# Kernel tuning notes

Measured on AMD Instinct MI355X. Metric: run time of the kernel, lower is better.

Reference implementation:

```python
import jax, jax.numpy as jnp
import numpy as np

D = 4
P_PIX = 13   # 2*R+1, R=6
R_PIX = 6
P_REG = 7    # R+1
DIRATE = 2   # min(4, (20-0)//15 + 1) for ref_index=[0,18], current_ind=20, dil_int=15


def correlate(t, r, P, d):
    """SpatialCorrelationSampler(kernel_size=1, patch_size=P, dilation_patch=d).
    t, r: [b,c,h,w] -> [b,P*P,h,w] ; corr[n=(i*P+j)] uses r shifted by ((i-R)*d,(j-R)*d)."""
    b, c, h, w = t.shape
    Rr = (P - 1) // 2
    pad = Rr * d
    rp = jnp.pad(r, ((0, 0), (0, 0), (pad, pad), (pad, pad)))
    # [b,c,N,h,w] stack of shifted views (zero-padded borders)
    shifts = jnp.stack([rp[:, :, i * d:i * d + h, j * d:j * d + w]
                        for i in range(P) for j in range(P)], axis=2)
    return jnp.einsum('bcyx,bcnyx->bnyx', t, shifts)


def deform_im2col(r, offset, P):
    """Deformable im2col with one shared (x,y) offset per output pixel.
    r: [b,c,h,w], offset: [b,h,w,2] (x in [...,0], y in [...,1]) -> [b,c,P*P,h,w].
    Bilinear sampling with zero outside the image."""
    b, c, h, w = r.shape
    Rr = (P - 1) // 2
    N = P * P
    ky, kx = jnp.meshgrid(jnp.arange(-Rr, Rr + 1), jnp.arange(-Rr, Rr + 1), indexing='ij')
    ky = ky.reshape(-1).astype(r.dtype)
    kx = kx.reshape(-1).astype(r.dtype)
    ys = jnp.arange(h, dtype=r.dtype)
    xs = jnp.arange(w, dtype=r.dtype)
    sy = offset[..., 1][:, None] + ys[None, None, :, None] + ky[None, :, None, None]  # [b,N,h,w]
    sx = offset[..., 0][:, None] + xs[None, None, None, :] + kx[None, :, None, None]
    y0 = jnp.floor(sy)
    x0 = jnp.floor(sx)
    wy = sy - y0
    wx = sx - x0
    rf = r.reshape(b, c, h * w)

    def gather(yi, xi):
        valid = ((yi >= 0) & (yi < h) & (xi >= 0) & (xi < w)).astype(r.dtype)
        idx = (jnp.clip(yi, 0, h - 1).astype(jnp.int32) * w
               + jnp.clip(xi, 0, w - 1).astype(jnp.int32)).reshape(b, 1, -1)
        vals = jnp.take_along_axis(rf, jnp.broadcast_to(idx, (b, c, N * h * w)), axis=2)
        return vals.reshape(b, c, N, h, w), valid

    v00, m00 = gather(y0, x0)
    v01, m01 = gather(y0, x0 + 1)
    v10, m10 = gather(y0 + 1, x0)
    v11, m11 = gather(y0 + 1, x0 + 1)
    w00 = ((1 - wy) * (1 - wx) * m00)[:, None]
    w01 = ((1 - wy) * wx * m01)[:, None]
    w10 = (wy * (1 - wx) * m10)[:, None]
    w11 = (wy * wx * m11)[:, None]
    return v00 * w00 + v01 * w01 + v10 * w10 + v11 * w11


def unfold(x, P):
    """F.unfold(x, kernel_size=P, padding=(P-1)//2) -> [b,c,P*P,h,w]."""
    b, c, h, w = x.shape
    Rr = (P - 1) // 2
    xp = jnp.pad(x, ((0, 0), (0, 0), (Rr, Rr), (Rr, Rr)))
    return jnp.stack([xp[:, :, i:i + h, j:j + w]
                      for i in range(P) for j in range(P)], axis=2)


def setup_inputs() -> dict:
    key = jax.random.key(0)
    ks = jax.random.split(key, 8)
    inp = {
        'feats_r0': jax.random.normal(ks[0], (2, 128, 32, 32), jnp.float32),
        'feats_r1': jax.random.normal(ks[1], (2, 128, 32, 32), jnp.float32),
        'feats_t': jax.random.normal(ks[2], (2, 128, 32, 32), jnp.float32),
        'quantized_r0': jax.random.uniform(ks[3], (2, 3, 128, 128), jnp.float32),
        'quantized_r1': jax.random.uniform(ks[4], (2, 3, 128, 128), jnp.float32),
        'feats_r_semantic0': jax.random.normal(ks[5], (2, 512, 16, 16), jnp.float32),
        'feats_r_semantic1': jax.random.normal(ks[6], (2, 512, 16, 16), jnp.float32),
        'feats_t_semantic': jax.random.normal(ks[7], (2, 512, 16, 16), jnp.float32),
        'current_ind': 20,
    }
    return inp


def reference(feats_r0, feats_r1, feats_t, quantized_r0, quantized_r1,
              feats_r_semantic0, feats_r_semantic1, feats_t_semantic, current_ind):
    b, c, h, w = feats_t.shape
    b_, c_, h_, w_ = feats_t_semantic.shape
    P, Rr, N = P_PIX, R_PIX, P_PIX * P_PIX

    # --- searching ref 0 (far in time): dilated coarse correlation -> soft offset ---
    coarse = correlate(feats_t, feats_r0, P, DIRATE)                     # [b,N,h,w]
    cs = jax.nn.softmax(coarse.reshape(b, N, h * w), axis=1).reshape(b, P, P, h, w)
    gv = jnp.arange(-Rr, Rr + 1, dtype=feats_t.dtype)
    off_x = jnp.einsum('bijyx,j->byx', cs, gv) * DIRATE
    off_y = jnp.einsum('bijyx,i->byx', cs, gv) * DIRATE
    offset = jnp.stack([off_x, off_y], axis=-1)                          # [b,h,w,2]

    col0 = deform_im2col(feats_r0, offset, P)                            # [b,c,N,h,w]
    corr0 = jnp.einsum('bcyx,bcnyx->bnyx', feats_t, col0).reshape(b, N, h * w)

    # --- recent ref 1: plain pixel + region correlation ---
    corr1 = correlate(feats_t, feats_r1, P, 1).reshape(b, N, h * w)
    region = correlate(feats_t_semantic, feats_r_semantic1, P_REG, 1).reshape(b_, P_REG * P_REG, h_ * w_)
    corr = jax.nn.softmax(region, axis=1)[:, None]                       # [b,1,49,h_*w_]

    corr_pixel = jax.nn.softmax(jnp.concatenate([corr0, corr1], axis=1), axis=1)[:, None]  # [b,1,2N,hw]

    # --- propagate colors ---
    qr0 = quantized_r0[:, :, ::D, ::D]
    qr1 = quantized_r1[:, :, ::D, ::D]
    uf0 = deform_im2col(qr0, offset, P).reshape(b, 3, N, h * w)
    uf1 = unfold(qr1, P).reshape(b, 3, N, h * w)
    image_uf = jnp.concatenate([uf0, uf1], axis=2)                       # [b,3,2N,hw]
    out = (corr_pixel * image_uf).sum(2).reshape(b, 3, h, w)
    return (out, corr)
```

## Files before the change

### kernel.cpp

```cpp
#include <hip/hip_runtime.h>
#include <math.h>

#define HH 32
#define WW 32
#define CC 128
#define PPIX 13
#define RPIX 6
#define NPIX 169
#define G14 14
#define NG 196
#define NTOT 338
#define DIRATE_ 2
#define HS 16
#define WSz 16
#define CS 512
#define PREG 7
#define RREG 3
#define NREG 49
#define QH 128
#define MAIN_BLOCKS 2048
#define REG_BLOCKS 512

__device__ __forceinline__ float wave_sum(float v) {
    #pragma unroll
    for (int s = 1; s < 64; s <<= 1) v += __shfl_xor(v, s, 64);
    return v;
}
__device__ __forceinline__ float wave_max(float v) {
    #pragma unroll
    for (int s = 1; s < 64; s <<= 1) v = fmaxf(v, __shfl_xor(v, s, 64));
    return v;
}

__global__ __launch_bounds__(256) void prep(
    const float* __restrict__ fr0, const float* __restrict__ fr1,
    const float* __restrict__ ft,  const float* __restrict__ qr0,
    const float* __restrict__ qr1, const float* __restrict__ rs1,
    const float* __restrict__ ts,
    float* __restrict__ Tr0, float* __restrict__ Tr1, float* __restrict__ Tt,
    float* __restrict__ Trs1, float* __restrict__ Tts,
    float* __restrict__ qs0, float* __restrict__ qs1)
{
    __shared__ float tile[32][33];
    const int tid = threadIdx.x;
    const int tx = tid & 31, ty = tid >> 5;
    int bid = blockIdx.x;
    if (bid < 768) {
        const int t = bid >> 8, rem = bid & 255;
        const int p0 = (rem & 31) * 32;
        const int c0 = ((rem >> 5) & 3) * 32;
        const int b  = rem >> 7;
        const float* s = (t==0 ? fr0 : t==1 ? fr1 : ft) + (size_t)b*CC*1024;
        float* d       = (t==0 ? Tr0 : t==1 ? Tr1 : Tt) + (size_t)b*CC*1024;
        #pragma unroll
        for (int i = ty; i < 32; i += 8) tile[i][tx] = s[(size_t)(c0+i)*1024 + p0+tx];
        __syncthreads();
        #pragma unroll
        for (int i = ty; i < 32; i += 8) d[(size_t)(p0+i)*CC + c0+tx] = tile[tx][i];
    } else if (bid < 1280) {
        bid -= 768;
        const int t = bid >> 8, rem = bid & 255;
        const int p0 = (rem & 7) * 32;
        const int c0 = ((rem >> 3) & 15) * 32;
        const int b  = rem >> 7;
        const float* s = (t==0 ? rs1 : ts) + (size_t)b*CS*256;
        float* d       = (t==0 ? Trs1 : Tts) + (size_t)b*CS*256;
        #pragma unroll
        for (int i = ty; i < 32; i += 8) tile[i][tx] = s[(size_t)(c0+i)*256 + p0+tx];
        __syncthreads();
        #pragma unroll
        for (int i = ty; i < 32; i += 8) d[(size_t)(p0+i)*CS + c0+tx] = tile[tx][i];
    } else {
        const int base = (bid - 1280) * 256 + tid;
        for (int e = base; e < 2*6144; e += 2048) {
            const int t = e / 6144, r2 = e % 6144;
            const int bc = r2 >> 10, yx = r2 & 1023;
            const int yy = yx >> 5, xx = yx & 31;
            const float v = (t==0 ? qr0 : qr1)[((size_t)bc*QH + yy*4)*QH + xx*4];
            (t==0 ? qs0 : qs1)[r2] = v;
        }
    }
}

__global__ __launch_bounds__(256) void colorizer_fused(
    const float* __restrict__ Tr0,
    const float* __restrict__ Tr1,
    const float* __restrict__ Tt,
    const float* __restrict__ qs0,
    const float* __restrict__ qs1,
    const float* __restrict__ Trs1,
    const float* __restrict__ Tts,
    float* __restrict__ out,
    float* __restrict__ corr_out)
{
    __shared__ __align__(16) float tvec[CS];
    __shared__ float rbuf[40];
    __shared__ float smC0[NPIX];
    __shared__ float smG[NG];
    __shared__ float smC1[NPIX];
    __shared__ float smV[NTOT];
    __shared__ float smQ0[3*NG];
    __shared__ float smQ1[3*NPIX];

    const int tid  = threadIdx.x;
    const int lane = tid & 63;
    const int wid  = tid >> 6;

    if (blockIdx.x < MAIN_BLOCKS) {
        const int b   = blockIdx.x >> 10;
        const int pix = blockIdx.x & 1023;
        const int y = pix >> 5, x = pix & 31;

        if (tid < 32)
            ((float4*)tvec)[tid] = ((const float4*)Tt)[(size_t)b*32768 + pix*32 + tid];
        __syncthreads();

        const float4* tp  = (const float4*)tvec;
        const float4* Tr0q = (const float4*)Tr0 + (size_t)b*32768;
        const float4* Tr1q = (const float4*)Tr1 + (size_t)b*32768;
        const int q4 = lane & 3, g4 = lane >> 2;

        #pragma unroll
        for (int set = 0; set < 3; ++set) {
            const int di = set*64 + wid*16 + g4;
            int inb = 0, yx = 0;
            if (di < NPIX) {
                const int ys = y + (di/PPIX - RPIX)*DIRATE_;
                const int xs = x + (di%PPIX - RPIX)*DIRATE_;
                inb = (ys>=0 && ys<HH && xs>=0 && xs<WW);
                yx = inb ? ys*WW+xs : 0;
            }
            const float4* rp = Tr0q + yx*32 + q4;
            float4 a; a.x=a.y=a.z=a.w=0.f;
            #pragma unroll
            for (int r = 0; r < 8; ++r) {
                const float4 rv = rp[r*4];
                const float4 tv = tp[q4 + r*4];
                a.x = fmaf(rv.x,tv.x,a.x); a.y = fmaf(rv.y,tv.y,a.y);
                a.z = fmaf(rv.z,tv.z,a.z); a.w = fmaf(rv.w,tv.w,a.w);
            }
            float s = (a.x+a.y)+(a.z+a.w);
            s += __shfl_xor(s, 1, 64); s += __shfl_xor(s, 2, 64);
            if (q4 == 0 && di < NPIX) smC0[di] = inb ? s : 0.f;
        }
        __syncthreads();

        const float dv = (tid < NPIX) ? smC0[tid] : 0.f;
        {
            float wm = wave_max(tid < NPIX ? dv : -INFINITY);
            if (lane == 0) rbuf[wid] = wm;
        }
        __syncthreads();
        const float M1 = fmaxf(fmaxf(rbuf[0], rbuf[1]), fmaxf(rbuf[2], rbuf[3]));
        {
            const float e   = (tid < NPIX) ? __expf(dv - M1) : 0.f;
            const float gvj = (tid < NPIX) ? (float)(tid % PPIX - RPIX) : 0.f;
            const float gvi = (tid < NPIX) ? (float)(tid / PPIX - RPIX) : 0.f;
            float s0 = wave_sum(e), s1 = wave_sum(e*gvj), s2 = wave_sum(e*gvi);
            if (lane == 0) { rbuf[4+wid] = s0; rbuf[8+wid] = s1; rbuf[12+wid] = s2; }
        }
        __syncthreads();
        const float ssum = rbuf[4]+rbuf[5]+rbuf[6]+rbuf[7];
        const float sx   = rbuf[8]+rbuf[9]+rbuf[10]+rbuf[11];
        const float sy   = rbuf[12]+rbuf[13]+rbuf[14]+rbuf[15];
        const float off_x = sx / ssum * (float)DIRATE_;
        const float off_y = sy / ssum * (float)DIRATE_;

        const float fy = (float)y + off_y, fx = (float)x + off_x;
        const float fly = floorf(fy), flx = floorf(fx);
        const int yb = (int)fly - RPIX, xb = (int)flx - RPIX;
        const float wy = fy - fly, wx = fx - flx;
        const float w00 = (1.f-wy)*(1.f-wx), w01 = (1.f-wy)*wx;
        const float w10 = wy*(1.f-wx),       w11 = wy*wx;

        #pragma unroll
        for (int set = 0; set < 6; ++set) {
            const int di = set*64 + wid*16 + g4;
            const float4* basep = Tr0q;
            int inb = 0, yx = 0;
            if (di < NG) {
                const int ys = yb + di/G14, xs = xb + di%G14;
                inb = (ys>=0 && ys<HH && xs>=0 && xs<WW);
                yx = inb ? ys*WW+xs : 0;
            } else if (di < NG+NPIX) {
                const int k = di - NG;
                const int ys = y + k/PPIX - RPIX, xs = x + k%PPIX - RPIX;
                inb = (ys>=0 && ys<HH && xs>=0 && xs<WW);
                yx = inb ? ys*WW+xs : 0;
                basep = Tr1q;
            }
            const float4* rp = basep + yx*32 + q4;
            float4 a; a.x=a.y=a.z=a.w=0.f;
            #pragma unroll
            for (int r = 0; r < 8; ++r) {
                const float4 rv = rp[r*4];
                const float4 tv = tp[q4 + r*4];
                a.x = fmaf(rv.x,tv.x,a.x); a.y = fmaf(rv.y,tv.y,a.y);
                a.z = fmaf(rv.z,tv.z,a.z); a.w = fmaf(rv.w,tv.w,a.w);
            }
            float s = (a.x+a.y)+(a.z+a.w);
            s += __shfl_xor(s, 1, 64); s += __shfl_xor(s, 2, 64);
            if (q4 == 0 && di < NG+NPIX) {
                if (di < NG) smG[di] = inb ? s : 0.f;
                else         smC1[di-NG] = inb ? s : 0.f;
            }
        }
        for (int idx = tid; idx < 3*NG; idx += 256) {
            const int ch = idx / NG, a2 = idx % NG;
            const int ys = yb + a2 / G14, xs = xb + a2 % G14;
            smQ0[idx] = (ys>=0 && ys<HH && xs>=0 && xs<WW)
                        ? qs0[(b*3+ch)*1024 + ys*WW + xs] : 0.f;
        }
        for (int idx = tid; idx < 3*NPIX; idx += 256) {
            const int ch = idx / NPIX, a2 = idx % NPIX;
            const int ys = y + a2 / PPIX - RPIX, xs = x + a2 % PPIX - RPIX;
            smQ1[idx] = (ys>=0 && ys<HH && xs>=0 && xs<WW)
                        ? qs1[(b*3+ch)*1024 + ys*WW + xs] : 0.f;
        }
        __syncthreads();

        for (int idx = tid; idx < NTOT; idx += 256) {
            float v;
            if (idx < NPIX) {
                const int i = idx / PPIX, j = idx % PPIX;
                const int g = i*G14 + j;
                v = w00*smG[g] + w01*smG[g+1] + w10*smG[g+G14] + w11*smG[g+G14+1];
            } else {
                v = smC1[idx - NPIX];
            }
            smV[idx] = v;
        }
        __syncthreads();

        float ml = -INFINITY;
        for (int idx = tid; idx < NTOT; idx += 256) ml = fmaxf(ml, smV[idx]);
        {
            float wm = wave_max(ml);
            if (lane == 0) rbuf[16+wid] = wm;
        }
        __syncthreads();
        const float M2 = fmaxf(fmaxf(rbuf[16], rbuf[17]), fmaxf(rbuf[18], rbuf[19]));

        float dpart = 0.f, o0 = 0.f, o1 = 0.f, o2 = 0.f;
        for (int idx = tid; idx < NTOT; idx += 256) {
            const float ee = __expf(smV[idx] - M2);
            dpart += ee;
            if (idx < NPIX) {
                const int i = idx / PPIX, j = idx % PPIX;
                const int g = i*G14 + j;
                o0 += ee * (w00*smQ0[g]          + w01*smQ0[g+1]
                          + w10*smQ0[g+G14]      + w11*smQ0[g+G14+1]);
                o1 += ee * (w00*smQ0[NG+g]       + w01*smQ0[NG+g+1]
                          + w10*smQ0[NG+g+G14]   + w11*smQ0[NG+g+G14+1]);
                o2 += ee * (w00*smQ0[2*NG+g]     + w01*smQ0[2*NG+g+1]
                          + w10*smQ0[2*NG+g+G14] + w11*smQ0[2*NG+g+G14+1]);
            } else {
                const int k = idx - NPIX;
                o0 += ee * smQ1[k];
                o1 += ee * smQ1[NPIX + k];
                o2 += ee * smQ1[2*NPIX + k];
            }
        }
        {
            float s0 = wave_sum(dpart), s1 = wave_sum(o0), s2 = wave_sum(o1), s3 = wave_sum(o2);
            if (lane == 0) { rbuf[20+wid]=s0; rbuf[24+wid]=s1; rbuf[28+wid]=s2; rbuf[32+wid]=s3; }
        }
        __syncthreads();
        if (tid == 0) {
            const float denom = rbuf[20]+rbuf[21]+rbuf[22]+rbuf[23];
            const float inv = 1.f / denom;
            out[((b*3+0)*HH + y)*WW + x] = (rbuf[24]+rbuf[25]+rbuf[26]+rbuf[27]) * inv;
            out[((b*3+1)*HH + y)*WW + x] = (rbuf[28]+rbuf[29]+rbuf[30]+rbuf[31]) * inv;
            out[((b*3+2)*HH + y)*WW + x] = (rbuf[32]+rbuf[33]+rbuf[34]+rbuf[35]) * inv;
        }
    } else {
        const int rb  = blockIdx.x - MAIN_BLOCKS;
        const int b   = rb >> 8;
        const int pix = rb & 255;
        const int y = pix >> 4, x = pix & 15;

        if (tid < 128)
            ((float4*)tvec)[tid] = ((const float4*)Tts)[(size_t)b*32768 + pix*128 + tid];
        __syncthreads();

        const float4* tp  = (const float4*)tvec;
        const float4* Tsq = (const float4*)Trs1 + (size_t)b*32768;
        const int q8 = lane & 7, g8 = lane >> 3;

        #pragma unroll
        for (int set = 0; set < 2; ++set) {
            const int di = set*32 + wid*8 + g8;
            int inb = 0, yx = 0;
            if (di < NREG) {
                const int ys = y + di/PREG - RREG, xs = x + di%PREG - RREG;
                inb = (ys>=0 && ys<HS && xs>=0 && xs<WSz);
                yx = inb ? ys*WSz+xs : 0;
            }
            const float4* rp = Tsq + yx*128 + q8;
            float4 a; a.x=a.y=a.z=a.w=0.f;
            #pragma unroll 8
            for (int r = 0; r < 16; ++r) {
                const float4 rv = rp[r*8];
                const float4 tv = tp[q8 + r*8];
                a.x = fmaf(rv.x,tv.x,a.x); a.y = fmaf(rv.y,tv.y,a.y);
                a.z = fmaf(rv.z,tv.z,a.z); a.w = fmaf(rv.w,tv.w,a.w);
            }
            float s = (a.x+a.y)+(a.z+a.w);
            s += __shfl_xor(s, 1, 64); s += __shfl_xor(s, 2, 64); s += __shfl_xor(s, 4, 64);
            if (q8 == 0 && di < NREG) smG[di] = inb ? s : 0.f;
        }
        __syncthreads();

        const bool act = tid < NREG;
        const float val = act ? smG[tid] : -INFINITY;
        {
            float wm = wave_max(val);
            if (lane == 0) rbuf[wid] = wm;
        }
        __syncthreads();
        const float M = fmaxf(fmaxf(rbuf[0], rbuf[1]), fmaxf(rbuf[2], rbuf[3]));
        const float e = act ? __expf(val - M) : 0.f;
        {
            float s0 = wave_sum(e);
            if (lane == 0) rbuf[4+wid] = s0;
        }
        __syncthreads();
        const float s = rbuf[4]+rbuf[5]+rbuf[6]+rbuf[7];
        if (act) corr_out[b*NREG*(HS*WSz) + tid*(HS*WSz) + pix] = e / s;
    }
}

extern "C" void kernel_launch(void* const* d_in, const int* in_sizes, int n_in,
                              void* d_out, int out_size, void* d_ws, size_t ws_size,
                              hipStream_t stream) {
    const float* feats_r0 = (const float*)d_in[0];
    const float* feats_r1 = (const float*)d_in[1];
    const float* feats_t  = (const float*)d_in[2];
    const float* q_r0     = (const float*)d_in[3];
    const float* q_r1     = (const float*)d_in[4];
    const float* rs1      = (const float*)d_in[6];
    const float* ts       = (const float*)d_in[7];

    float* ws = (float*)d_ws;
    float* Tr0  = ws;
    float* Tr1  = Tr0  + 262144;
    float* Tt   = Tr1  + 262144;
    float* Trs1 = Tt   + 262144;
    float* Tts  = Trs1 + 262144;
    float* qs0  = Tts  + 262144;
    float* qs1  = qs0  + 6144;

    prep<<<1288, 256, 0, stream>>>(feats_r0, feats_r1, feats_t, q_r0, q_r1,
                                   rs1, ts, Tr0, Tr1, Tt, Trs1, Tts, qs0, qs1);

    float* out  = (float*)d_out;
    float* corr = out + 2*3*HH*WW;

    colorizer_fused<<<MAIN_BLOCKS + REG_BLOCKS, 256, 0, stream>>>(
        Tr0, Tr1, Tt, qs0, qs1, Trs1, Tts, out, corr);
}
```

Before: 102.0 us.

## Cache target vector in registers, swizzle block order, regroup region lanes

Each thread now loads its slice of the target feature vector from shared memory into registers once and reuses it across all displacement sets, instead of re-reading it from LDS in every set. The loops over sets are no longer unrolled, to limit register pressure. Block indices are interleaved in strides of eight for both main and region blocks, which changes which pixels run at the same time and so which neighbour data is shared in cache. The region branch regroups each wave to 16 lanes per displacement with 8 float4 loads per lane, adding one more shuffle step to the reduction.

Result: faster. 99.63 us (-2.3%).

```diff
diff --git a/kernel.cpp b/kernel.cpp
--- a/kernel.cpp
+++ b/kernel.cpp
@@ -107,8 +107,9 @@
     const int wid  = tid >> 6;
 
     if (blockIdx.x < MAIN_BLOCKS) {
-        const int b   = blockIdx.x >> 10;
-        const int pix = blockIdx.x & 1023;
+        const int bid = (blockIdx.x & 7) * (MAIN_BLOCKS/8) + (blockIdx.x >> 3);
+        const int b   = bid >> 10;
+        const int pix = bid & 1023;
         const int y = pix >> 5, x = pix & 31;
 
         if (tid < 32)
@@ -120,7 +121,11 @@
         const float4* Tr1q = (const float4*)Tr1 + (size_t)b*32768;
         const int q4 = lane & 3, g4 = lane >> 2;
 
-        #pragma unroll
+        float4 tf[8];
+        #pragma unroll
+        for (int r = 0; r < 8; ++r) tf[r] = tp[q4 + r*4];
+
+        #pragma unroll 1
         for (int set = 0; set < 3; ++set) {
             const int di = set*64 + wid*16 + g4;
             int inb = 0, yx = 0;
@@ -135,9 +140,8 @@
             #pragma unroll
             for (int r = 0; r < 8; ++r) {
                 const float4 rv = rp[r*4];
-                const float4 tv = tp[q4 + r*4];
-                a.x = fmaf(rv.x,tv.x,a.x); a.y = fmaf(rv.y,tv.y,a.y);
-                a.z = fmaf(rv.z,tv.z,a.z); a.w = fmaf(rv.w,tv.w,a.w);
+                a.x = fmaf(rv.x,tf[r].x,a.x); a.y = fmaf(rv.y,tf[r].y,a.y);
+                a.z = fmaf(rv.z,tf[r].z,a.z); a.w = fmaf(rv.w,tf[r].w,a.w);
             }
             float s = (a.x+a.y)+(a.z+a.w);
             s += __shfl_xor(s, 1, 64); s += __shfl_xor(s, 2, 64);
@@ -173,7 +177,7 @@
         const float w00 = (1.f-wy)*(1.f-wx), w01 = (1.f-wy)*wx;
         const float w10 = wy*(1.f-wx),       w11 = wy*wx;
 
-        #pragma unroll
+        #pragma unroll 1
         for (int set = 0; set < 6; ++set) {
             const int di = set*64 + wid*16 + g4;
             const float4* basep = Tr0q;
@@ -194,9 +198,8 @@
             #pragma unroll
             for (int r = 0; r < 8; ++r) {
                 const float4 rv = rp[r*4];
-                const float4 tv = tp[q4 + r*4];
-                a.x = fmaf(rv.x,tv.x,a.x); a.y = fmaf(rv.y,tv.y,a.y);
-                a.z = fmaf(rv.z,tv.z,a.z); a.w = fmaf(rv.w,tv.w,a.w);
+                a.x = fmaf(rv.x,tf[r].x,a.x); a.y = fmaf(rv.y,tf[r].y,a.y);
+                a.z = fmaf(rv.z,tf[r].z,a.z); a.w = fmaf(rv.w,tf[r].w,a.w);
             }
             float s = (a.x+a.y)+(a.z+a.w);
             s += __shfl_xor(s, 1, 64); s += __shfl_xor(s, 2, 64);
@@ -274,7 +277,8 @@
             out[((b*3+2)*HH + y)*WW + x] = (rbuf[32]+rbuf[33]+rbuf[34]+rbuf[35]) * inv;
         }
     } else {
-        const int rb  = blockIdx.x - MAIN_BLOCKS;
+        const int rb0 = blockIdx.x - MAIN_BLOCKS;
+        const int rb  = (rb0 & 7) * (REG_BLOCKS/8) + (rb0 >> 3);
         const int b   = rb >> 8;
         const int pix = rb & 255;
         const int y = pix >> 4, x = pix & 15;
@@ -285,29 +289,33 @@
 
         const float4* tp  = (const float4*)tvec;
         const float4* Tsq = (const float4*)Trs1 + (size_t)b*32768;
-        const int q8 = lane & 7, g8 = lane >> 3;
-
-        #pragma unroll
-        for (int set = 0; set < 2; ++set) {
-            const int di = set*32 + wid*8 + g8;
+        const int q16 = lane & 15, g16 = lane >> 4;
+
+        float4 tf[8];
+        #pragma unroll
+        for (int r = 0; r < 8; ++r) tf[r] = tp[q16 + r*16];
+
+        #pragma unroll 1
+        for (int set = 0; set < 4; ++set) {
+            const int di = set*16 + wid*4 + g16;
             int inb = 0, yx = 0;
             if (di < NREG) {
                 const int ys = y + di/PREG - RREG, xs = x + di%PREG - RREG;
                 inb = (ys>=0 && ys<HS && xs>=0 && xs<WSz);
                 yx = inb ? ys*WSz+xs : 0;
             }
-            const float4* rp = Tsq + yx*128 + q8;
+            const float4* rp = Tsq + yx*128 + q16;
             float4 a; a.x=a.y=a.z=a.w=0.f;
-            #pragma unroll 8
-            for (int r = 0; r < 16; ++r) {
-                const float4 rv = rp[r*8];
-                const float4 tv = tp[q8 + r*8];
-                a.x = fmaf(rv.x,tv.x,a.x); a.y = fmaf(rv.y,tv.y,a.y);
-                a.z = fmaf(rv.z,tv.z,a.z); a.w = fmaf(rv.w,tv.w,a.w);
+            #pragma unroll
+            for (int r = 0; r < 8; ++r) {
+                const float4 rv = rp[r*16];
+                a.x = fmaf(rv.x,tf[r].x,a.x); a.y = fmaf(rv.y,tf[r].y,a.y);
+                a.z = fmaf(rv.z,tf[r].z,a.z); a.w = fmaf(rv.w,tf[r].w,a.w);
             }
             float s = (a.x+a.y)+(a.z+a.w);
-            s += __shfl_xor(s, 1, 64); s += __shfl_xor(s, 2, 64); s += __shfl_xor(s, 4, 64);
-            if (q8 == 0 && di < NREG) smG[di] = inb ? s : 0.f;
+            s += __shfl_xor(s, 1, 64); s += __shfl_xor(s, 2, 64);
+            s += __shfl_xor(s, 4, 64); s += __shfl_xor(s, 8, 64);
+            if (q16 == 0 && di < NREG) smG[di] = inb ? s : 0.f;
         }
         __syncthreads();
 
```

## Use 512-thread blocks, register-cache target vector, and swizzle block order

Applied to the files above, without the earlier changes.

Doubles the block size of the fused colorizer kernel to 512 threads. Each wave now handles fewer correlation sets, and the softmax and color passes drop their strided loops because one thread covers one element. The target feature slice is cached in registers instead of being reread from shared memory, and the region blocks are scheduled first. Block indices are swizzled by 8, probably to spread neighbouring pixels across XCDs/L2. The region path is reduced to a single wave-level softmax. In exchange, the larger blocks raise register pressure and may lower occupancy, and more threads sit idle in the small region blocks.

Measured after the change: 112.6 us. 1.1x slower.

```diff
diff --git a/kernel.cpp b/kernel.cpp
--- a/kernel.cpp
+++ b/kernel.cpp
@@ -82,7 +82,7 @@
     }
 }
 
-__global__ __launch_bounds__(256) void colorizer_fused(
+__global__ __launch_bounds__(512) void colorizer_fused(
     const float* __restrict__ Tr0,
     const float* __restrict__ Tr1,
     const float* __restrict__ Tt,
@@ -94,7 +94,7 @@
     float* __restrict__ corr_out)
 {
     __shared__ __align__(16) float tvec[CS];
-    __shared__ float rbuf[40];
+    __shared__ float rbuf[72];
     __shared__ float smC0[NPIX];
     __shared__ float smG[NG];
     __shared__ float smC1[NPIX];
@@ -106,9 +106,11 @@
     const int lane = tid & 63;
     const int wid  = tid >> 6;
 
-    if (blockIdx.x < MAIN_BLOCKS) {
-        const int b   = blockIdx.x >> 10;
-        const int pix = blockIdx.x & 1023;
+    if (blockIdx.x >= REG_BLOCKS) {
+        const int orig = blockIdx.x - REG_BLOCKS;
+        const int bid = (orig & 7) * (MAIN_BLOCKS/8) + (orig >> 3);
+        const int b   = bid >> 10;
+        const int pix = bid & 1023;
         const int y = pix >> 5, x = pix & 31;
 
         if (tid < 32)
@@ -120,9 +122,13 @@
         const float4* Tr1q = (const float4*)Tr1 + (size_t)b*32768;
         const int q4 = lane & 3, g4 = lane >> 2;
 
-        #pragma unroll
-        for (int set = 0; set < 3; ++set) {
-            const int di = set*64 + wid*16 + g4;
+        float4 tf[8];
+        #pragma unroll
+        for (int r = 0; r < 8; ++r) tf[r] = tp[q4 + r*4];
+
+        #pragma unroll 1
+        for (int set = 0; set < 2; ++set) {
+            const int di = set*128 + wid*16 + g4;
             int inb = 0, yx = 0;
             if (di < NPIX) {
                 const int ys = y + (di/PPIX - RPIX)*DIRATE_;
@@ -135,9 +141,8 @@
             #pragma unroll
             for (int r = 0; r < 8; ++r) {
                 const float4 rv = rp[r*4];
-                const float4 tv = tp[q4 + r*4];
-                a.x = fmaf(rv.x,tv.x,a.x); a.y = fmaf(rv.y,tv.y,a.y);
-                a.z = fmaf(rv.z,tv.z,a.z); a.w = fmaf(rv.w,tv.w,a.w);
+                a.x = fmaf(rv.x,tf[r].x,a.x); a.y = fmaf(rv.y,tf[r].y,a.y);
+                a.z = fmaf(rv.z,tf[r].z,a.z); a.w = fmaf(rv.w,tf[r].w,a.w);
             }
             float s = (a.x+a.y)+(a.z+a.w);
             s += __shfl_xor(s, 1, 64); s += __shfl_xor(s, 2, 64);
@@ -151,18 +156,20 @@
             if (lane == 0) rbuf[wid] = wm;
         }
         __syncthreads();
-        const float M1 = fmaxf(fmaxf(rbuf[0], rbuf[1]), fmaxf(rbuf[2], rbuf[3]));
+        float M1 = rbuf[0];
+        #pragma unroll
+        for (int i = 1; i < 8; ++i) M1 = fmaxf(M1, rbuf[i]);
         {
             const float e   = (tid < NPIX) ? __expf(dv - M1) : 0.f;
             const float gvj = (tid < NPIX) ? (float)(tid % PPIX - RPIX) : 0.f;
             const float gvi = (tid < NPIX) ? (float)(tid / PPIX - RPIX) : 0.f;
             float s0 = wave_sum(e), s1 = wave_sum(e*gvj), s2 = wave_sum(e*gvi);
-            if (lane == 0) { rbuf[4+wid] = s0; rbuf[8+wid] = s1; rbuf[12+wid] = s2; }
-        }
-        __syncthreads();
-        const float ssum = rbuf[4]+rbuf[5]+rbuf[6]+rbuf[7];
-        const float sx   = rbuf[8]+rbuf[9]+rbuf[10]+rbuf[11];
-        const float sy   = rbuf[12]+rbuf[13]+rbuf[14]+rbuf[15];
+            if (lane == 0) { rbuf[8+wid] = s0; rbuf[16+wid] = s1; rbuf[24+wid] = s2; }
+        }
+        __syncthreads();
+        float ssum = 0.f, sx = 0.f, sy = 0.f;
+        #pragma unroll
+        for (int i = 0; i < 8; ++i) { ssum += rbuf[8+i]; sx += rbuf[16+i]; sy += rbuf[24+i]; }
         const float off_x = sx / ssum * (float)DIRATE_;
         const float off_y = sy / ssum * (float)DIRATE_;
 
@@ -173,9 +180,9 @@
         const float w00 = (1.f-wy)*(1.f-wx), w01 = (1.f-wy)*wx;
         const float w10 = wy*(1.f-wx),       w11 = wy*wx;
 
-        #pragma unroll
-        for (int set = 0; set < 6; ++set) {
-            const int di = set*64 + wid*16 + g4;
+        #pragma unroll 1
+        for (int set = 0; set < 3; ++set) {
+            const int di = set*128 + wid*16 + g4;
             const float4* basep = Tr0q;
             int inb = 0, yx = 0;
             if (di < NG) {
@@ -194,9 +201,8 @@
             #pragma unroll
             for (int r = 0; r < 8; ++r) {
                 const float4 rv = rp[r*4];
-                const float4 tv = tp[q4 + r*4];
-                a.x = fmaf(rv.x,tv.x,a.x); a.y = fmaf(rv.y,tv.y,a.y);
-                a.z = fmaf(rv.z,tv.z,a.z); a.w = fmaf(rv.w,tv.w,a.w);
+                a.x = fmaf(rv.x,tf[r].x,a.x); a.y = fmaf(rv.y,tf[r].y,a.y);
+                a.z = fmaf(rv.z,tf[r].z,a.z); a.w = fmaf(rv.w,tf[r].w,a.w);
             }
             float s = (a.x+a.y)+(a.z+a.w);
             s += __shfl_xor(s, 1, 64); s += __shfl_xor(s, 2, 64);
@@ -205,13 +211,13 @@
                 else         smC1[di-NG] = inb ? s : 0.f;
             }
         }
-        for (int idx = tid; idx < 3*NG; idx += 256) {
+        for (int idx = tid; idx < 3*NG; idx += 512) {
             const int ch = idx / NG, a2 = idx % NG;
             const int ys = yb + a2 / G14, xs = xb + a2 % G14;
             smQ0[idx] = (ys>=0 && ys<HH && xs>=0 && xs<WW)
                         ? qs0[(b*3+ch)*1024 + ys*WW + xs] : 0.f;
         }
-        for (int idx = tid; idx < 3*NPIX; idx += 256) {
+        for (int idx = tid; idx < 3*NPIX; idx += 512) {
             const int ch = idx / NPIX, a2 = idx % NPIX;
             const int ys = y + a2 / PPIX - RPIX, xs = x + a2 % PPIX - RPIX;
             smQ1[idx] = (ys>=0 && ys<HH && xs>=0 && xs<WW)
@@ -219,62 +225,68 @@
         }
         __syncthreads();
 
-        for (int idx = tid; idx < NTOT; idx += 256) {
+        if (tid < NTOT) {
             float v;
-            if (idx < NPIX) {
-                const int i = idx / PPIX, j = idx % PPIX;
+            if (tid < NPIX) {
+                const int i = tid / PPIX, j = tid % PPIX;
                 const int g = i*G14 + j;
                 v = w00*smG[g] + w01*smG[g+1] + w10*smG[g+G14] + w11*smG[g+G14+1];
             } else {
-                v = smC1[idx - NPIX];
-            }
-            smV[idx] = v;
-        }
-        __syncthreads();
-
-        float ml = -INFINITY;
-        for (int idx = tid; idx < NTOT; idx += 256) ml = fmaxf(ml, smV[idx]);
+                v = smC1[tid - NPIX];
+            }
+            smV[tid] = v;
+        }
+        __syncthreads();
+
+        const float ml = (tid < NTOT) ? smV[tid] : -INFINITY;
         {
             float wm = wave_max(ml);
-            if (lane == 0) rbuf[16+wid] = wm;
-        }
-        __syncthreads();
-        const float M2 = fmaxf(fmaxf(rbuf[16], rbuf[17]), fmaxf(rbuf[18], rbuf[19]));
+            if (lane == 0) rbuf[32+wid] = wm;
+        }
+        __syncthreads();
+        float M2 = rbuf[32];
+        #pragma unroll
+        for (int i = 1; i < 8; ++i) M2 = fmaxf(M2, rbuf[32+i]);
 
         float dpart = 0.f, o0 = 0.f, o1 = 0.f, o2 = 0.f;
-        for (int idx = tid; idx < NTOT; idx += 256) {
-            const float ee = __expf(smV[idx] - M2);
-            dpart += ee;
-            if (idx < NPIX) {
-                const int i = idx / PPIX, j = idx % PPIX;
+        if (tid < NTOT) {
+            const float ee = __expf(ml - M2);
+            dpart = ee;
+            if (tid < NPIX) {
+                const int i = tid / PPIX, j = tid % PPIX;
                 const int g = i*G14 + j;
-                o0 += ee * (w00*smQ0[g]          + w01*smQ0[g+1]
-                          + w10*smQ0[g+G14]      + w11*smQ0[g+G14+1]);
-                o1 += ee * (w00*smQ0[NG+g]       + w01*smQ0[NG+g+1]
-                          + w10*smQ0[NG+g+G14]   + w11*smQ0[NG+g+G14+1]);
-                o2 += ee * (w00*smQ0[2*NG+g]     + w01*smQ0[2*NG+g+1]
-                          + w10*smQ0[2*NG+g+G14] + w11*smQ0[2*NG+g+G14+1]);
+                o0 = ee * (w00*smQ0[g]          + w01*smQ0[g+1]
+                         + w10*smQ0[g+G14]      + w11*smQ0[g+G14+1]);
+                o1 = ee * (w00*smQ0[NG+g]       + w01*smQ0[NG+g+1]
+                         + w10*smQ0[NG+g+G14]   + w11*smQ0[NG+g+G14+1]);
+                o2 = ee * (w00*smQ0[2*NG+g]     + w01*smQ0[2*NG+g+1]
+                         + w10*smQ0[2*NG+g+G14] + w11*smQ0[2*NG+g+G14+1]);
             } else {
-                const int k = idx - NPIX;
-                o0 += ee * smQ1[k];
-                o1 += ee * smQ1[NPIX + k];
-                o2 += ee * smQ1[2*NPIX + k];
+                const int k = tid - NPIX;
+                o0 = ee * smQ1[k];
+                o1 = ee * smQ1[NPIX + k];
+                o2 = ee * smQ1[2*NPIX + k];
             }
         }
         {
             float s0 = wave_sum(dpart), s1 = wave_sum(o0), s2 = wave_sum(o1), s3 = wave_sum(o2);
-            if (lane == 0) { rbuf[20+wid]=s0; rbuf[24+wid]=s1; rbuf[28+wid]=s2; rbuf[32+wid]=s3; }
+            if (lane == 0) { rbuf[40+wid]=s0; rbuf[48+wid]=s1; rbuf[56+wid]=s2; rbuf[64+wid]=s3; }
         }
         __syncthreads();
         if (tid == 0) {
-            const float denom = rbuf[20]+rbuf[21]+rbuf[22]+rbuf[23];
+            float denom=0.f, r0s=0.f, r1s=0.f, r2s=0.f;
+            #pragma unroll
+            for (int i = 0; i < 8; ++i) {
+                denom += rbuf[40+i]; r0s += rbuf[48+i]; r1s += rbuf[56+i]; r2s += rbuf[64+i];
+            }
             const float inv = 1.f / denom;
-            out[((b*3+0)*HH + y)*WW + x] = (rbuf[24]+rbuf[25]+rbuf[26]+rbuf[27]) * inv;
-            out[((b*3+1)*HH + y)*WW + x] = (rbuf[28]+rbuf[29]+rbuf[30]+rbuf[31]) * inv;
-            out[((b*3+2)*HH + y)*WW + x] = (rbuf[32]+rbuf[33]+rbuf[34]+rbuf[35]) * inv;
+            out[((b*3+0)*HH + y)*WW + x] = r0s * inv;
+            out[((b*3+1)*HH + y)*WW + x] = r1s * inv;
+            out[((b*3+2)*HH + y)*WW + x] = r2s * inv;
         }
     } else {
-        const int rb  = blockIdx.x - MAIN_BLOCKS;
+        const int rb0 = blockIdx.x;
+        const int rb  = (rb0 & 7) * (REG_BLOCKS/8) + (rb0 >> 3);
         const int b   = rb >> 8;
         const int pix = rb & 255;
         const int y = pix >> 4, x = pix & 15;
@@ -287,46 +299,35 @@
         const float4* Tsq = (const float4*)Trs1 + (size_t)b*32768;
         const int q8 = lane & 7, g8 = lane >> 3;
 
-        #pragma unroll
-        for (int set = 0; set < 2; ++set) {
-            const int di = set*32 + wid*8 + g8;
-            int inb = 0, yx = 0;
-            if (di < NREG) {
-                const int ys = y + di/PREG - RREG, xs = x + di%PREG - RREG;
-                inb = (ys>=0 && ys<HS && xs>=0 && xs<WSz);
-                yx = inb ? ys*WSz+xs : 0;
-            }
-            const float4* rp = Tsq + yx*128 + q8;
-            float4 a; a.x=a.y=a.z=a.w=0.f;
-            #pragma unroll 8
-            for (int r = 0; r < 16; ++r) {
-                const float4 rv = rp[r*8];
-                const float4 tv = tp[q8 + r*8];
-                a.x = fmaf(rv.x,tv.x,a.x); a.y = fmaf(rv.y,tv.y,a.y);
-                a.z = fmaf(rv.z,tv.z,a.z); a.w = fmaf(rv.w,tv.w,a.w);
-            }
-            float s = (a.x+a.y)+(a.z+a.w);
-            s += __shfl_xor(s, 1, 64); s += __shfl_xor(s, 2, 64); s += __shfl_xor(s, 4, 64);
-            if (q8 == 0 && di < NREG) smG[di] = inb ? s : 0.f;
-        }
-        __syncthreads();
-
-        const bool act = tid < NREG;
-        const float val = act ? smG[tid] : -INFINITY;
-        {
-            float wm = wave_max(val);
-            if (lane == 0) rbuf[wid] = wm;
-        }
-        __syncthreads();
-        const float M = fmaxf(fmaxf(rbuf[0], rbuf[1]), fmaxf(rbuf[2], rbuf[3]));
-        const float e = act ? __expf(val - M) : 0.f;
-        {
-            float s0 = wave_sum(e);
-            if (lane == 0) rbuf[4+wid] = s0;
-        }
-        __syncthreads();
-        const float s = rbuf[4]+rbuf[5]+rbuf[6]+rbuf[7];
-        if (act) corr_out[b*NREG*(HS*WSz) + tid*(HS*WSz) + pix] = e / s;
+        const int di = wid*8 + g8;
+        int inb = 0, yx = 0;
+        if (di < NREG) {
+            const int ys = y + di/PREG - RREG, xs = x + di%PREG - RREG;
+            inb = (ys>=0 && ys<HS && xs>=0 && xs<WSz);
+            yx = inb ? ys*WSz+xs : 0;
+        }
+        const float4* rp = Tsq + yx*128 + q8;
+        float4 a; a.x=a.y=a.z=a.w=0.f;
+        #pragma unroll 8
+        for (int r = 0; r < 16; ++r) {
+            const float4 rv = rp[r*8];
+            const float4 tv = tp[q8 + r*8];
+            a.x = fmaf(rv.x,tv.x,a.x); a.y = fmaf(rv.y,tv.y,a.y);
+            a.z = fmaf(rv.z,tv.z,a.z); a.w = fmaf(rv.w,tv.w,a.w);
+        }
+        float s = (a.x+a.y)+(a.z+a.w);
+        s += __shfl_xor(s, 1, 64); s += __shfl_xor(s, 2, 64); s += __shfl_xor(s, 4, 64);
+        if (q8 == 0 && di < NREG) smG[di] = inb ? s : 0.f;
+        __syncthreads();
+
+        if (wid == 0) {
+            const bool act = lane < NREG;
+            const float val = act ? smG[lane] : -INFINITY;
+            const float M = wave_max(val);
+            const float e = act ? __expf(val - M) : 0.f;
+            const float ssum = wave_sum(e);
+            if (act) corr_out[b*NREG*(HS*WSz) + lane*(HS*WSz) + pix] = e / ssum;
+        }
     }
 }
 
@@ -356,6 +357,6 @@
     float* out  = (float*)d_out;
     float* corr = out + 2*3*HH*WW;
 
-    colorizer_fused<<<MAIN_BLOCKS + REG_BLOCKS, 256, 0, stream>>>(
+    colorizer_fused<<<MAIN_BLOCKS + REG_BLOCKS, 512, 0, stream>>>(
         Tr0, Tr1, Tt, qs0, qs1, Trs1, Tts, out, corr);
 }
```
